# Kernel optimization log

Hardware: AMD Instinct MI355X
Metric: run time of the kernel (lower is better)

Reference implementation:

```python
import jax, jax.numpy as jnp
import numpy as np

HIDDEN = 5120
NH = 32
DQ = 128    # qk nope dim
DR = 64     # qk rope dim
DV = 128    # v head dim
Q_LORA = 1536
KV_LORA = 512
T = 2048
THETA = 10000.0
EPS = 1e-6


def rmsnorm(x, g, eps=EPS):
    return x * jax.lax.rsqrt(jnp.mean(x * x, axis=-1, keepdims=True) + eps) * g


def rotate_gptj(x):
    # interleaved pairs: (x0, x1) -> (-x1, x0)
    x1 = x[..., ::2]
    x2 = x[..., 1::2]
    return jnp.stack((-x2, x1), axis=-1).reshape(x.shape)


def setup_inputs() -> dict:
    key = jax.random.key(0)
    ks = jax.random.split(key, 8)
    s = 0.02
    return {
        'positions': jnp.arange(T, dtype=jnp.int32),
        'hidden_states': jax.random.normal(ks[0], (T, HIDDEN), jnp.float32),
        'w_qa': jax.random.normal(ks[1], (HIDDEN, Q_LORA), jnp.float32) * s,
        'gamma_q': jnp.ones((Q_LORA,), jnp.float32),
        'w_qb': jax.random.normal(ks[2], (Q_LORA, NH * (DQ + DR)), jnp.float32) * s,
        'w_kva': jax.random.normal(ks[3], (HIDDEN, KV_LORA + DR), jnp.float32) * s,
        'gamma_kv': jnp.ones((KV_LORA,), jnp.float32),
        'w_kvb': jax.random.normal(ks[4], (KV_LORA, NH * (DQ + DV)), jnp.float32) * s,
        'w_o': jax.random.normal(ks[5], (NH * DV, HIDDEN), jnp.float32) * s,
    }


def reference(positions, hidden_states, w_qa, gamma_q, w_qb, w_kva, gamma_kv, w_kvb, w_o):
    t = hidden_states.shape[0]
    # --- Q path: low-rank down-proj, RMSNorm, up-proj ---
    q_c = rmsnorm(hidden_states @ w_qa, gamma_q)               # [T, Q_LORA]
    q = (q_c @ w_qb).reshape(t, NH, DQ + DR)                   # [T, H, 192]
    q_nope, q_pe = q[..., :DQ], q[..., DQ:]
    # --- KV path: joint down-proj, split latent / rope key, RMSNorm latent ---
    kv = hidden_states @ w_kva                                 # [T, KV_LORA + DR]
    kv_c, k_pe = kv[:, :KV_LORA], kv[:, KV_LORA:]
    kv_c = rmsnorm(kv_c, gamma_kv)
    kv_up = (kv_c @ w_kvb).reshape(t, NH, DQ + DV)             # [T, H, 256]
    k_nope, v = kv_up[..., :DQ], kv_up[..., DQ:]
    # --- partial RoPE (GPT-J rotate, neox-style cos/sin cache) ---
    inv_freq = 1.0 / (THETA ** (jnp.arange(0, DR, 2, dtype=jnp.float32) / DR))
    freqs = positions.astype(jnp.float32)[:, None] * inv_freq  # [T, DR/2]
    emb = jnp.concatenate((freqs, freqs), axis=-1)             # [T, DR]
    cos = jnp.cos(emb)[:, None, :]                             # [T, 1, DR]
    sin = jnp.sin(emb)[:, None, :]
    q_pe = q_pe * cos + rotate_gptj(q_pe) * sin                # [T, H, DR]
    k_pe = k_pe[:, None, :]
    k_pe = k_pe * cos + rotate_gptj(k_pe) * sin                # [T, 1, DR]
    # --- attention ---
    q_full = jnp.concatenate((q_nope, q_pe), axis=-1)                          # [T, H, 192]
    k_full = jnp.concatenate((k_nope, jnp.broadcast_to(k_pe, (t, NH, DR))), axis=-1)
    scale = (DQ + DR) ** -0.5
    scores = jnp.einsum('qhd,khd->hqk', q_full, k_full) * scale                # [H, T, T]
    causal = positions[:, None] >= positions[None, :]
    scores = jnp.where(causal[None], scores, jnp.float32(-1e30))
    attn = jax.nn.softmax(scores, axis=-1)
    out = jnp.einsum('hqk,khd->qhd', attn, v).reshape(t, NH * DV)              # [T, H*DV]
    return out @ w_o                                                           # [T, HIDDEN]
```

## Files before the change

kernel.cpp:

```cpp
#include <hip/hip_runtime.h>
#include <hip/hip_bf16.h>
#include <cstdint>
#include <cstddef>

#define T_SEQ   2048
#define HIDDEN  5120
#define NH      32
#define DQ      128
#define DR      64
#define DV      128
#define Q_LORA  1536
#define KV_LORA 512
#define QD      (DQ + DR)
#define KVD     (KV_LORA + DR)
#define QROW    (NH * QD)
#define KVUPROW (NH * (DQ + DV))
#define AOROW   (NH * DV)
#define FUSED_N (Q_LORA + KVD)
#define FUSED_PE (Q_LORA + KV_LORA)

typedef short bf16x8 __attribute__((ext_vector_type(8)));
typedef float f32x4  __attribute__((ext_vector_type(4)));

#define GLOAD16(gp, lp)                                                        \
    __builtin_amdgcn_global_load_lds(                                          \
        (const __attribute__((address_space(1))) void*)(gp),                   \
        (__attribute__((address_space(3))) void*)(lp), 16, 0, 0)

static __device__ __forceinline__ short f2bf(float f)
{
    union { float f; unsigned u; } v; v.f = f;
    unsigned r = v.u + 0x7FFFu + ((v.u >> 16) & 1u);
    return (short)(r >> 16);
}
static __device__ __forceinline__ float bf2f(short s)
{
    union { unsigned u; float f; } v;
    v.u = ((unsigned)(unsigned short)s) << 16;
    return v.f;
}

__global__ __launch_bounds__(256) void zero_f32(float* __restrict__ p, int n4)
{
    const int stride = gridDim.x * 256;
    for (int i = blockIdx.x * 256 + threadIdx.x; i < n4; i += stride)
        ((float4*)p)[i] = make_float4(0.f, 0.f, 0.f, 0.f);
}

__global__ __launch_bounds__(256) void conv_bf(
    const float* __restrict__ src, short* __restrict__ dst)
{
    const size_t i = ((size_t)blockIdx.x * 256 + threadIdx.x) * 8;
    float4 a = *(const float4*)&src[i];
    float4 b = *(const float4*)&src[i + 4];
    union { short s[8]; uint4 u; } o;
    o.s[0] = f2bf(a.x); o.s[1] = f2bf(a.y); o.s[2] = f2bf(a.z); o.s[3] = f2bf(a.w);
    o.s[4] = f2bf(b.x); o.s[5] = f2bf(b.y); o.s[6] = f2bf(b.z); o.s[7] = f2bf(b.w);
    *(uint4*)&dst[i] = o.u;
}

__global__ __launch_bounds__(256) void tr_f32_bf16(
    const float* __restrict__ src, short* __restrict__ dst, int K, int N)
{
    const int k0 = blockIdx.x * 32, n0 = blockIdx.y * 32;
    __shared__ float t[32][33];
    const int tid = threadIdx.x;
    {
        const int r = tid >> 3, c4 = (tid & 7) * 4;
        float4 v = *(const float4*)&src[(size_t)(k0 + r) * N + n0 + c4];
        t[r][c4 + 0] = v.x; t[r][c4 + 1] = v.y;
        t[r][c4 + 2] = v.z; t[r][c4 + 3] = v.w;
    }
    __syncthreads();
    {
        const int n = tid >> 3, k4 = (tid & 7) * 4;
        union { short s[4]; uint2 u; } o;
#pragma unroll
        for (int j = 0; j < 4; ++j) o.s[j] = f2bf(t[k4 + j][n]);
        *(uint2*)&dst[(size_t)(n0 + n) * K + k0 + k4] = o.u;
    }
}

__global__ __launch_bounds__(256, 4) void gemm_bt(
    const short* __restrict__ A, const short* __restrict__ BT,
    float* __restrict__ Cf, short* __restrict__ Cb, int N, int K,
    int lda, int ldbt, int ldc)
{
    __shared__ short As[128 * 64];
    __shared__ short Bs[128 * 64];

    const int gx = gridDim.x;
    const int nwg = gx * gridDim.y;
    int flat = blockIdx.y * gx + blockIdx.x;
    if ((nwg & 7) == 0) {
        const int chunk = nwg >> 3;
        flat = (flat & 7) * chunk + (flat >> 3);
    }
    const int bm = (flat / gx) * 128;
    const int bn = (flat % gx) * 128;

    const int kchunk = K / gridDim.z;
    const int kbeg   = kchunk * blockIdx.z;
    const int kend   = kbeg + kchunk;

    const int tid  = threadIdx.x;
    const int w    = tid >> 6;
    const int l    = tid & 63;
    const int wm   = (w >> 1) * 64;
    const int wn   = (w & 1) * 64;
    const int quad = l >> 4;
    const int lrow = l & 15;

    f32x4 acc[4][4];
#pragma unroll
    for (int mt = 0; mt < 4; ++mt)
#pragma unroll
        for (int nt = 0; nt < 4; ++nt)
            acc[mt][nt] = (f32x4){0.f, 0.f, 0.f, 0.f};

    const int r0  = tid >> 3;
    const int c8  = (tid & 7) * 8;
    const int rbA = bm + r0;
    int rbB = bn + r0; if (rbB > N - 1) rbB = N - 1;

    for (int k0 = kbeg; k0 < kend; k0 += 64) {
        __syncthreads();
#pragma unroll
        for (int i = 0; i < 4; ++i) {
            const int r = r0 + 32 * i;
            GLOAD16(&A[(size_t)(rbA + 32 * i) * lda + k0 + c8], &As[r * 64 + c8]);
        }
#pragma unroll
        for (int i = 0; i < 4; ++i) {
            const int r  = r0 + 32 * i;
            int rb = rbB + 32 * i; if (rb > N - 1) rb = N - 1;
            GLOAD16(&BT[(size_t)rb * ldbt + k0 + c8], &Bs[r * 64 + c8]);
        }
        __syncthreads();

#pragma unroll
        for (int ks = 0; ks < 2; ++ks) {
            bf16x8 af[4], bfr[4];
#pragma unroll
            for (int mt = 0; mt < 4; ++mt)
                af[mt] = *(const bf16x8*)&As[(wm + mt * 16 + lrow) * 64 + ks * 32 + quad * 8];
#pragma unroll
            for (int nt = 0; nt < 4; ++nt)
                bfr[nt] = *(const bf16x8*)&Bs[(wn + nt * 16 + lrow) * 64 + ks * 32 + quad * 8];
#pragma unroll
            for (int mt = 0; mt < 4; ++mt)
#pragma unroll
                for (int nt = 0; nt < 4; ++nt)
                    acc[mt][nt] = __builtin_amdgcn_mfma_f32_16x16x32_bf16(
                        af[mt], bfr[nt], acc[mt][nt], 0, 0, 0);
        }
    }

    if (Cb == nullptr) {
        const bool atom = (gridDim.z > 1);
#pragma unroll
        for (int mt = 0; mt < 4; ++mt)
#pragma unroll
            for (int i = 0; i < 4; ++i) {
                const int row = bm + wm + mt * 16 + quad * 4 + i;
                float* crow = Cf + (size_t)row * ldc;
#pragma unroll
                for (int nt = 0; nt < 4; ++nt) {
                    const int col = bn + wn + nt * 16 + lrow;
                    if (col < N) {
                        if (atom) atomicAdd(&crow[col], acc[mt][nt][i]);
                        else      crow[col] = acc[mt][nt][i];
                    }
                }
            }
    } else {
#pragma unroll
        for (int mt = 0; mt < 4; ++mt)
#pragma unroll
            for (int i = 0; i < 4; ++i) {
                const int row = bm + wm + mt * 16 + quad * 4 + i;
                short* crow = Cb + (size_t)row * ldc;
#pragma unroll
                for (int nt = 0; nt < 4; ++nt) {
                    const int col = bn + wn + nt * 16 + lrow;
                    if (col < N) crow[col] = f2bf(acc[mt][nt][i]);
                }
            }
    }
}

__global__ __launch_bounds__(256, 4) void gemm_kv(
    const short* __restrict__ A, const short* __restrict__ BT,
    short* __restrict__ Kg, short* __restrict__ Vg)
{
    __shared__ short As[128 * 64];
    __shared__ short Bs[128 * 64];

    const int gx = gridDim.x;
    const int nwg = gx * gridDim.y;
    int flat = blockIdx.y * gx + blockIdx.x;
    if ((nwg & 7) == 0) {
        const int chunk = nwg >> 3;
        flat = (flat & 7) * chunk + (flat >> 3);
    }
    const int bm = (flat / gx) * 128;
    const int bn = (flat % gx) * 128;

    const int tid  = threadIdx.x;
    const int w    = tid >> 6;
    const int l    = tid & 63;
    const int wm   = (w >> 1) * 64;
    const int wn   = (w & 1) * 64;
    const int quad = l >> 4;
    const int lrow = l & 15;

    f32x4 acc[4][4];
#pragma unroll
    for (int mt = 0; mt < 4; ++mt)
#pragma unroll
        for (int nt = 0; nt < 4; ++nt)
            acc[mt][nt] = (f32x4){0.f, 0.f, 0.f, 0.f};

    const int r0 = tid >> 3;
    const int c8 = (tid & 7) * 8;

    for (int k0 = 0; k0 < KV_LORA; k0 += 64) {
        __syncthreads();
#pragma unroll
        for (int i = 0; i < 4; ++i) {
            const int r = r0 + 32 * i;
            GLOAD16(&A[(size_t)(bm + r) * KV_LORA + k0 + c8], &As[r * 64 + c8]);
        }
#pragma unroll
        for (int i = 0; i < 4; ++i) {
            const int r = r0 + 32 * i;
            GLOAD16(&BT[(size_t)(bn + r) * KV_LORA + k0 + c8], &Bs[r * 64 + c8]);
        }
        __syncthreads();

#pragma unroll
        for (int ks = 0; ks < 2; ++ks) {
            bf16x8 af[4], bfr[4];
#pragma unroll
            for (int mt = 0; mt < 4; ++mt)
                af[mt] = *(const bf16x8*)&As[(wm + mt * 16 + lrow) * 64 + ks * 32 + quad * 8];
#pragma unroll
            for (int nt = 0; nt < 4; ++nt)
                bfr[nt] = *(const bf16x8*)&Bs[(wn + nt * 16 + lrow) * 64 + ks * 32 + quad * 8];
#pragma unroll
            for (int mt = 0; mt < 4; ++mt)
#pragma unroll
                for (int nt = 0; nt < 4; ++nt)
                    acc[mt][nt] = __builtin_amdgcn_mfma_f32_16x16x32_bf16(
                        af[mt], bfr[nt], acc[mt][nt], 0, 0, 0);
        }
    }

    const int  h     = bn >> 8;
    const bool vhalf = (bn & 128) != 0;
    if (!vhalf) {
        short* KgH = Kg + (size_t)h * (2048 * 192);
#pragma unroll
        for (int mt = 0; mt < 4; ++mt)
#pragma unroll
            for (int i = 0; i < 4; ++i) {
                const int row = bm + wm + mt * 16 + quad * 4 + i;
#pragma unroll
                for (int nt = 0; nt < 4; ++nt) {
                    const int d = wn + nt * 16 + lrow;
                    KgH[(size_t)row * 192 + d] = f2bf(acc[mt][nt][i]);
                }
            }
    } else {
        short* VgH = Vg + (size_t)h * (128 * 2048);
#pragma unroll
        for (int mt = 0; mt < 4; ++mt)
#pragma unroll
            for (int nt = 0; nt < 4; ++nt) {
                const int dv   = wn + nt * 16 + lrow;
                const int rowb = bm + wm + mt * 16 + quad * 4;
                union { short s[4]; uint2 u; } t;
                t.s[0] = f2bf(acc[mt][nt][0]); t.s[1] = f2bf(acc[mt][nt][1]);
                t.s[2] = f2bf(acc[mt][nt][2]); t.s[3] = f2bf(acc[mt][nt][3]);
                *(uint2*)&VgH[(size_t)dv * 2048 + rowb] = t.u;
            }
    }
}

__global__ __launch_bounds__(256) void rmsnorm_bf(
    const float* __restrict__ x, const float* __restrict__ g,
    short* __restrict__ y, int len, int in_stride, int out_stride)
{
    const float* xr = x + (size_t)blockIdx.x * in_stride;
    short*       yr = y + (size_t)blockIdx.x * out_stride;
    float ss = 0.f;
    for (int i = threadIdx.x; i < len; i += 256) {
        float v = xr[i];
        ss += v * v;
    }
#pragma unroll
    for (int off = 32; off > 0; off >>= 1) ss += __shfl_down(ss, off);
    __shared__ float red[4];
    if ((threadIdx.x & 63) == 0) red[threadIdx.x >> 6] = ss;
    __syncthreads();
    float tot = red[0] + red[1] + red[2] + red[3];
    float scale = rsqrtf(tot / (float)len + 1e-6f);
    for (int i = threadIdx.x; i < len; i += 256)
        yr[i] = f2bf(xr[i] * scale * g[i]);
}

#define ROPE_LN_THETA_OVER_32 0.28782313662425575f

__device__ __forceinline__ void rope_pair(float p, int i, float& x0, float& x1)
{
    const int   j0 = (2 * i) & 31;
    const int   j1 = (2 * i + 1) & 31;
    const float a0 = p * expf(-(float)j0 * ROPE_LN_THETA_OVER_32);
    const float a1 = p * expf(-(float)j1 * ROPE_LN_THETA_OVER_32);
    const float r0 = x0 * cosf(a0) - x1 * sinf(a0);
    const float r1 = x1 * cosf(a1) + x0 * sinf(a1);
    x0 = r0; x1 = r1;
}

__global__ __launch_bounds__(256) void rope_q_bf(
    short* __restrict__ qb, const int* __restrict__ pos)
{
    const int idx = blockIdx.x * 256 + threadIdx.x;
    const int i = idx & 31;
    const int h = (idx >> 5) & 31;
    const int t = idx >> 10;
    short* base = qb + (size_t)t * QROW + h * QD + DQ;
    float x0 = bf2f(base[2 * i]), x1 = bf2f(base[2 * i + 1]);
    rope_pair((float)pos[t], i, x0, x1);
    union { short s[2]; unsigned u; } o;
    o.s[0] = f2bf(x0); o.s[1] = f2bf(x1);
    *(unsigned*)&base[2 * i] = o.u;
}

__global__ __launch_bounds__(256) void rope_k_bcast(
    const float* __restrict__ qkva, const int* __restrict__ pos,
    short* __restrict__ Kg)
{
    const int idx = blockIdx.x * 256 + threadIdx.x;
    const int i = idx & 31;
    const int t = idx >> 5;
    const float* base = qkva + (size_t)t * FUSED_N + FUSED_PE;
    float x0 = base[2 * i], x1 = base[2 * i + 1];
    rope_pair((float)pos[t], i, x0, x1);
    union { short s[2]; unsigned u; } pk;
    pk.s[0] = f2bf(x0); pk.s[1] = f2bf(x1);
    for (int h = 0; h < NH; ++h)
        *(unsigned*)&Kg[((size_t)h * 2048 + t) * 192 + 128 + 2 * i] = pk.u;
}

__global__ __launch_bounds__(256) void attn_mfma(
    const short* __restrict__ qb, const short* __restrict__ Kg,
    const short* __restrict__ Vg, short* __restrict__ aout)
{
    const int h   = blockIdx.x;
    const int qb_ = gridDim.y - 1 - blockIdx.y;
    const int q0  = qb_ * 64;

    __shared__ short Ks[64 * 200];
    __shared__ short Vt[128 * 72];
    __shared__ short Ps[64 * 72];

    const int tid  = threadIdx.x;
    const int w    = tid >> 6;
    const int l    = tid & 63;
    const int quad = l >> 4;
    const int lrow = l & 15;

    const float K2 = 0.104117547f;

    bf16x8 afq[6];
    {
        const short* qrow = qb + (size_t)(q0 + w * 16 + lrow) * QROW + h * QD;
#pragma unroll
        for (int ks = 0; ks < 6; ++ks)
            afq[ks] = *(const bf16x8*)&qrow[ks * 32 + quad * 8];
    }

    f32x4 Oacc[8];
#pragma unroll
    for (int nt = 0; nt < 8; ++nt) Oacc[nt] = (f32x4){0.f, 0.f, 0.f, 0.f};
    float m_run[4] = {-1e30f, -1e30f, -1e30f, -1e30f};
    float l_run[4] = {0.f, 0.f, 0.f, 0.f};

    const short* KgH = Kg + (size_t)h * (2048 * 192);
    const short* VgH = Vg + (size_t)h * (128 * 2048);

    uint4 kreg[6], vreg[4];
#pragma unroll
    for (int it = 0; it < 6; ++it) {
        const int id = tid + 256 * it;
        const int r = id / 24, g = id % 24;
        kreg[it] = *(const uint4*)&KgH[(size_t)r * 192 + g * 8];
    }
#pragma unroll
    for (int it = 0; it < 4; ++it) {
        const int id = tid + 256 * it;
        const int rv = id >> 3, g = id & 7;
        vreg[it] = *(const uint4*)&VgH[(size_t)rv * 2048 + g * 8];
    }

    for (int kt = 0; kt <= qb_; ++kt) {
        __syncthreads();
#pragma unroll
        for (int it = 0; it < 6; ++it) {
            const int id = tid + 256 * it;
            const int r = id / 24, g = id % 24;
            *(uint4*)&Ks[r * 200 + g * 8] = kreg[it];
        }
#pragma unroll
        for (int it = 0; it < 4; ++it) {
            const int id = tid + 256 * it;
            const int rv = id >> 3, g = id & 7;
            *(uint4*)&Vt[rv * 72 + g * 8] = vreg[it];
        }
        __syncthreads();

        if (kt < qb_) {
#pragma unroll
            for (int it = 0; it < 6; ++it) {
                const int id = tid + 256 * it;
                const int r = id / 24, g = id % 24;
                kreg[it] = *(const uint4*)&KgH[(size_t)((kt + 1) * 64 + r) * 192 + g * 8];
            }
#pragma unroll
            for (int it = 0; it < 4; ++it) {
                const int id = tid + 256 * it;
                const int rv = id >> 3, g = id & 7;
                vreg[it] = *(const uint4*)&VgH[(size_t)rv * 2048 + (kt + 1) * 64 + g * 8];
            }
        }

        f32x4 Sc[4];
#pragma unroll
        for (int nt = 0; nt < 4; ++nt) Sc[nt] = (f32x4){0.f, 0.f, 0.f, 0.f};
#pragma unroll
        for (int ks = 0; ks < 6; ++ks)
#pragma unroll
            for (int nt = 0; nt < 4; ++nt) {
                bf16x8 bk = *(const bf16x8*)&Ks[(nt * 16 + lrow) * 200 + ks * 32 + quad * 8];
                Sc[nt] = __builtin_amdgcn_mfma_f32_16x16x32_bf16(afq[ks], bk, Sc[nt], 0, 0, 0);
            }

        if (kt == qb_) {
            const int qrow = w * 16 + quad * 4;
#pragma unroll
            for (int nt = 0; nt < 4; ++nt)
#pragma unroll
                for (int i = 0; i < 4; ++i)
                    if (nt * 16 + lrow > qrow + i) Sc[nt][i] = -1e30f;
        }

        float alpha[4], negmk[4];
#pragma unroll
        for (int i = 0; i < 4; ++i) {
            float m = fmaxf(fmaxf(Sc[0][i], Sc[1][i]), fmaxf(Sc[2][i], Sc[3][i]));
            m = fmaxf(m, __shfl_xor(m, 1));
            m = fmaxf(m, __shfl_xor(m, 2));
            m = fmaxf(m, __shfl_xor(m, 4));
            m = fmaxf(m, __shfl_xor(m, 8));
            const float mn = fmaxf(m_run[i], m);
            negmk[i] = -mn * K2;
            alpha[i] = exp2f(fmaf(m_run[i], K2, negmk[i]));
            m_run[i] = mn;
        }

        float rs[4] = {0.f, 0.f, 0.f, 0.f};
#pragma unroll
        for (int nt = 0; nt < 4; ++nt)
#pragma unroll
            for (int i = 0; i < 4; ++i) {
                const float p = exp2f(fmaf(Sc[nt][i], K2, negmk[i]));
                rs[i] += p;
                Ps[(w * 16 + quad * 4 + i) * 72 + nt * 16 + lrow] = f2bf(p);
            }
#pragma unroll
        for (int i = 0; i < 4; ++i) {
            float r = rs[i];
            r += __shfl_xor(r, 1);
            r += __shfl_xor(r, 2);
            r += __shfl_xor(r, 4);
            r += __shfl_xor(r, 8);
            l_run[i] = l_run[i] * alpha[i] + r;
        }

#pragma unroll
        for (int nt = 0; nt < 8; ++nt)
#pragma unroll
            for (int i = 0; i < 4; ++i) Oacc[nt][i] *= alpha[i];

#pragma unroll
        for (int ks2 = 0; ks2 < 2; ++ks2) {
            bf16x8 ap = *(const bf16x8*)&Ps[(w * 16 + lrow) * 72 + ks2 * 32 + quad * 8];
#pragma unroll
            for (int nt = 0; nt < 8; ++nt) {
                bf16x8 bv = *(const bf16x8*)&Vt[(nt * 16 + lrow) * 72 + ks2 * 32 + quad * 8];
                Oacc[nt] = __builtin_amdgcn_mfma_f32_16x16x32_bf16(ap, bv, Oacc[nt], 0, 0, 0);
            }
        }
    }

    float invl[4];
#pragma unroll
    for (int i = 0; i < 4; ++i) invl[i] = 1.f / l_run[i];
#pragma unroll
    for (int nt = 0; nt < 8; ++nt)
#pragma unroll
        for (int i = 0; i < 4; ++i)
            aout[(size_t)(q0 + w * 16 + quad * 4 + i) * AOROW + h * 128 + nt * 16 + lrow]
                = f2bf(Oacc[nt][i] * invl[i]);
}

extern "C" void kernel_launch(void* const* d_in, const int* in_sizes, int n_in,
                              void* d_out, int out_size, void* d_ws, size_t ws_size,
                              hipStream_t stream)
{
    const int*   positions = (const int*)d_in[0];
    const float* hidden    = (const float*)d_in[1];
    const float* w_qa      = (const float*)d_in[2];
    const float* gamma_q   = (const float*)d_in[3];
    const float* w_qb      = (const float*)d_in[4];
    const float* w_kva     = (const float*)d_in[5];
    const float* gamma_kv  = (const float*)d_in[6];
    const float* w_kvb     = (const float*)d_in[7];
    const float* w_o       = (const float*)d_in[8];
    float*       out       = (float*)d_out;

    short* wT      = (short*)d_ws;
    short* hid_bf  = wT      + (size_t)20971520;
    short* qbuf_bf = hid_bf  + (size_t)T_SEQ * HIDDEN;
    short* Kg      = qbuf_bf + (size_t)T_SEQ * QROW;
    short* Vg      = Kg      + (size_t)NH * 2048 * 192;
    short* aout_bf = Vg      + (size_t)NH * 128 * 2048;
    short* qa_bf   = aout_bf + (size_t)T_SEQ * AOROW;
    short* kvc_bf  = qa_bf   + (size_t)T_SEQ * Q_LORA;
    float* qkva    = (float*)Vg;

    const dim3 blk(256);

    zero_f32<<<dim3(2048), blk, 0, stream>>>(qkva, T_SEQ * FUSED_N / 4);
    zero_f32<<<dim3(2048), blk, 0, stream>>>(out, T_SEQ * HIDDEN / 4);
    conv_bf<<<dim3(T_SEQ * HIDDEN / 8 / 256), blk, 0, stream>>>(hidden, hid_bf);

    tr_f32_bf16<<<dim3(HIDDEN / 32, Q_LORA / 32), blk, 0, stream>>>(w_qa, wT, HIDDEN, Q_LORA);
    tr_f32_bf16<<<dim3(HIDDEN / 32, KVD / 32), blk, 0, stream>>>(
        w_kva, wT + (size_t)Q_LORA * HIDDEN, HIDDEN, KVD);
    gemm_bt<<<dim3((FUSED_N + 127) / 128, T_SEQ / 128, 2), blk, 0, stream>>>(
        hid_bf, wT, qkva, nullptr, FUSED_N, HIDDEN, HIDDEN, HIDDEN, FUSED_N);

    rmsnorm_bf<<<dim3(T_SEQ), blk, 0, stream>>>(qkva, gamma_q, qa_bf, Q_LORA, FUSED_N, Q_LORA);
    rmsnorm_bf<<<dim3(T_SEQ), blk, 0, stream>>>(qkva + Q_LORA, gamma_kv, kvc_bf,
                                                KV_LORA, FUSED_N, KV_LORA);
    rope_k_bcast<<<dim3(T_SEQ * 32 / 256), blk, 0, stream>>>(qkva, positions, Kg);

    tr_f32_bf16<<<dim3(Q_LORA / 32, QROW / 32), blk, 0, stream>>>(w_qb, wT, Q_LORA, QROW);
    gemm_bt<<<dim3(QROW / 128, T_SEQ / 128, 1), blk, 0, stream>>>(
        qa_bf, wT, nullptr, qbuf_bf, QROW, Q_LORA, Q_LORA, Q_LORA, QROW);

    tr_f32_bf16<<<dim3(KV_LORA / 32, KVUPROW / 32), blk, 0, stream>>>(w_kvb, wT, KV_LORA, KVUPROW);
    gemm_kv<<<dim3(KVUPROW / 128, T_SEQ / 128), blk, 0, stream>>>(kvc_bf, wT, Kg, Vg);

    rope_q_bf<<<dim3(T_SEQ * NH * 32 / 256), blk, 0, stream>>>(qbuf_bf, positions);

    attn_mfma<<<dim3(NH, T_SEQ / 64), blk, 0, stream>>>(qbuf_bf, Kg, Vg, aout_bf);

    tr_f32_bf16<<<dim3(AOROW / 32, HIDDEN / 32), blk, 0, stream>>>(w_o, wT, AOROW, HIDDEN);
    gemm_bt<<<dim3(HIDDEN / 128, T_SEQ / 128, 2), blk, 0, stream>>>(
        aout_bf, wT, out, nullptr, HIDDEN, AOROW, AOROW, AOROW, HIDDEN);
}
```

Before: 841.0 us.

## Load attention K/V tiles directly into swizzled LDS instead of register prefetch

The attention kernel drops its register-staged prefetch of the next K/V tile. Each iteration now issues direct global-to-LDS 16-byte loads through the GLOAD16 macro. The padded LDS rows (200 and 72 shorts) become unpadded rows with an XOR swizzle on the column, and the MFMA operand reads apply the same swizzle. The aim is to cut register pressure, skip the register-to-LDS copy, and avoid bank conflicts with less LDS. The cost is that the explicit overlap of the next tile's global loads with the current tile's compute is gone, so load latency may be exposed.

```diff
diff --git a/kernel.cpp b/kernel.cpp
--- a/kernel.cpp
+++ b/kernel.cpp
@@ -361,8 +361,8 @@
     const int qb_ = gridDim.y - 1 - blockIdx.y;
     const int q0  = qb_ * 64;
 
-    __shared__ short Ks[64 * 200];
-    __shared__ short Vt[128 * 72];
+    __shared__ short Ks[64 * 192];
+    __shared__ short Vt[128 * 64];
     __shared__ short Ps[64 * 72];
 
     const int tid  = threadIdx.x;
@@ -390,51 +390,24 @@
     const short* KgH = Kg + (size_t)h * (2048 * 192);
     const short* VgH = Vg + (size_t)h * (128 * 2048);
 
-    uint4 kreg[6], vreg[4];
-#pragma unroll
-    for (int it = 0; it < 6; ++it) {
-        const int id = tid + 256 * it;
-        const int r = id / 24, g = id % 24;
-        kreg[it] = *(const uint4*)&KgH[(size_t)r * 192 + g * 8];
-    }
-#pragma unroll
-    for (int it = 0; it < 4; ++it) {
-        const int id = tid + 256 * it;
-        const int rv = id >> 3, g = id & 7;
-        vreg[it] = *(const uint4*)&VgH[(size_t)rv * 2048 + g * 8];
-    }
-
     for (int kt = 0; kt <= qb_; ++kt) {
         __syncthreads();
 #pragma unroll
         for (int it = 0; it < 6; ++it) {
             const int id = tid + 256 * it;
             const int r = id / 24, g = id % 24;
-            *(uint4*)&Ks[r * 200 + g * 8] = kreg[it];
+            const int sc = (g * 8) ^ ((r & 7) << 3);
+            GLOAD16(&KgH[(size_t)(kt * 64 + r) * 192 + sc], &Ks[id * 8]);
         }
 #pragma unroll
         for (int it = 0; it < 4; ++it) {
             const int id = tid + 256 * it;
             const int rv = id >> 3, g = id & 7;
-            *(uint4*)&Vt[rv * 72 + g * 8] = vreg[it];
+            const int sc = (g * 8) ^ ((rv & 7) << 3);
+            GLOAD16(&VgH[(size_t)rv * 2048 + kt * 64 + sc], &Vt[id * 8]);
         }
         __syncthreads();
 
-        if (kt < qb_) {
-#pragma unroll
-            for (int it = 0; it < 6; ++it) {
-                const int id = tid + 256 * it;
-                const int r = id / 24, g = id % 24;
-                kreg[it] = *(const uint4*)&KgH[(size_t)((kt + 1) * 64 + r) * 192 + g * 8];
-            }
-#pragma unroll
-            for (int it = 0; it < 4; ++it) {
-                const int id = tid + 256 * it;
-                const int rv = id >> 3, g = id & 7;
-                vreg[it] = *(const uint4*)&VgH[(size_t)rv * 2048 + (kt + 1) * 64 + g * 8];
-            }
-        }
-
         f32x4 Sc[4];
 #pragma unroll
         for (int nt = 0; nt < 4; ++nt) Sc[nt] = (f32x4){0.f, 0.f, 0.f, 0.f};
@@ -442,7 +415,9 @@
         for (int ks = 0; ks < 6; ++ks)
 #pragma unroll
             for (int nt = 0; nt < 4; ++nt) {
-                bf16x8 bk = *(const bf16x8*)&Ks[(nt * 16 + lrow) * 200 + ks * 32 + quad * 8];
+                const int row = nt * 16 + lrow;
+                const int col = (ks * 32 + quad * 8) ^ ((row & 7) << 3);
+                bf16x8 bk = *(const bf16x8*)&Ks[row * 192 + col];
                 Sc[nt] = __builtin_amdgcn_mfma_f32_16x16x32_bf16(afq[ks], bk, Sc[nt], 0, 0, 0);
             }
 
@@ -498,7 +473,9 @@
             bf16x8 ap = *(const bf16x8*)&Ps[(w * 16 + lrow) * 72 + ks2 * 32 + quad * 8];
 #pragma unroll
             for (int nt = 0; nt < 8; ++nt) {
-                bf16x8 bv = *(const bf16x8*)&Vt[(nt * 16 + lrow) * 72 + ks2 * 32 + quad * 8];
+                const int row = nt * 16 + lrow;
+                const int col = (ks2 * 32 + quad * 8) ^ ((row & 7) << 3);
+                bf16x8 bv = *(const bf16x8*)&Vt[row * 64 + col];
                 Oacc[nt] = __builtin_amdgcn_mfma_f32_16x16x32_bf16(ap, bv, Oacc[nt], 0, 0, 0);
             }
         }
```

Result: faster. 710.2 us (-15.6%).
